# Performance work log

Measured on AMD Instinct MI355X. Metric: run time of the kernel, lower is better.

The kernel has to match this reference:

```python
import jax, jax.numpy as jnp
import numpy as np

N = 100000   # nodes
E = 3200000  # edges (avg degree 32)
F = 128      # feature dim
K = 10       # propagation order (hardcoded in module)


def setup_inputs() -> dict:
    key = jax.random.key(0)
    k1, k2 = jax.random.split(key, 2)
    x = jax.random.normal(k1, (N, F), dtype=jnp.float32)
    edge_index = jax.random.randint(k2, (2, E), 0, N, dtype=jnp.int32)
    mf_weights = jnp.ones((1, K + 1, 1), dtype=jnp.float32)
    # coef_upd='none' with alpha=0.5 -> lap_coefs init = min(1/0.5, 1.0) = 1.0, frozen
    lap_coefs = jnp.ones((K + 1,), dtype=jnp.float32)
    return {"x": x, "mf_weights": mf_weights, "lap_coefs": lap_coefs,
            "edge_index": edge_index}


def reference(x, mf_weights, lap_coefs, edge_index):
    n = x.shape[0]
    row, col = edge_index[0], edge_index[1]
    # gcn_norm without self loops: deg over destination (col), symmetric norm
    deg = jax.ops.segment_sum(jnp.ones((edge_index.shape[1],), x.dtype), col,
                              num_segments=n)
    dinv = jnp.where(deg > 0, jax.lax.rsqrt(jnp.maximum(deg, 1.0)) * jnp.where(deg > 0, jnp.ones_like(deg), 0.0), 0.0)
    dinv = jnp.where(deg > 0, deg ** -0.5, 0.0)
    norm = dinv[row] * dinv[col]  # [E]

    def prop(h):  # out[col] += norm * h[row]  (scatter-add SpMM)
        return jax.ops.segment_sum(norm[:, None] * h[row], col, num_segments=n)

    # Chebyshev-like recurrence: An=2, Bn=0, Cn=-1 -> P_i = 2*prop(P_{i-1}) - P_{i-2}
    outs = [x, prop(x)]
    for i in range(2, K + 1):
        outs.append(2.0 * prop(outs[-1]) - outs[-2])

    # coef_outs[0] = P0/1 ; coef_outs[i] = lap_coefs[i-1]/1 * P_i (norm_weights all 1)
    coef = jnp.concatenate([jnp.ones((1,), x.dtype), lap_coefs[:K]])  # [K+1]
    stacked = jnp.stack(outs, axis=1)  # [N, K+1, F]
    ret = jnp.sum(stacked * coef[None, :, None] * mf_weights, axis=1)  # [N, F]
    return ret
```

## Files before the change

kernel.cpp:

```cpp
#include <hip/hip_runtime.h>
#include <hip/hip_bf16.h>
#include <hip/hip_fp16.h>

#define FDIM 128


__global__ void degree_kernel(const int* __restrict__ col, int* __restrict__ deg, int E) {
    int e = blockIdx.x * blockDim.x + threadIdx.x;
    if (e < E) atomicAdd(&deg[col[e]], 1);
}

__global__ void dinv_kernel(const int* __restrict__ deg, float* __restrict__ dinv, int N) {
    int i = blockIdx.x * blockDim.x + threadIdx.x;
    if (i < N) {
        int d = deg[i];
        dinv[i] = (d > 0) ? rsqrtf((float)d) : 0.0f;
    }
}


__global__ void scan_blocks_kernel(const int* __restrict__ deg, int* __restrict__ rowptr,
                                   int* __restrict__ bsum, int N) {
    __shared__ int s[256];
    int t = threadIdx.x;
    int i = blockIdx.x * 256 + t;
    int v = (i < N) ? deg[i] : 0;
    s[t] = v;
    __syncthreads();
    for (int off = 1; off < 256; off <<= 1) {
        int add = (t >= off) ? s[t - off] : 0;
        __syncthreads();
        s[t] += add;
        __syncthreads();
    }
    if (i < N) rowptr[i] = s[t] - v;
    if (t == 255) bsum[blockIdx.x] = s[255];
}

__global__ void scan_bsums_kernel(int* __restrict__ bsum, int* __restrict__ boff, int nb) {
    __shared__ int s[512];
    int t = threadIdx.x;
    int v = (t < nb) ? bsum[t] : 0;
    s[t] = v;
    __syncthreads();
    for (int off = 1; off < 512; off <<= 1) {
        int add = (t >= off) ? s[t - off] : 0;
        __syncthreads();
        s[t] += add;
        __syncthreads();
    }
    if (t < nb) boff[t] = s[t] - v;
}

__global__ void add_offsets_kernel(int* __restrict__ rowptr, int* __restrict__ cursor,
                                   const int* __restrict__ boff, int N, int E) {
    int i = blockIdx.x * blockDim.x + threadIdx.x;
    if (i < N) {
        int v = rowptr[i] + boff[i >> 8];
        rowptr[i] = v;
        cursor[i] = v;
    }
    if (i == 0) rowptr[N] = E;
}


__global__ void place_kernel(const int* __restrict__ row, const int* __restrict__ col,
                             const float* __restrict__ dinv, int* __restrict__ cursor,
                             float2* __restrict__ edata, int E) {
    int e = blockIdx.x * blockDim.x + threadIdx.x;
    if (e < E) {
        int r = row[e], c = col[e];
        float w = dinv[r] * dinv[c];
        int pos = atomicAdd(&cursor[c], 1);
        edata[pos] = make_float2(__int_as_float(r), w);
    }
}


__global__ void init_out_kernel(const float4* __restrict__ x, const float* __restrict__ mf,
                                float4* __restrict__ out, long n4) {
    long i = (long)blockIdx.x * blockDim.x + threadIdx.x;
    if (i < n4) {
        float w = mf[0];
        float4 v = x[i];
        out[i] = make_float4(w * v.x, w * v.y, w * v.z, w * v.w);
    }
}


template <typename ST>
__global__ __launch_bounds__(256) void gather_prop_kernel(
        const float2* __restrict__ edata, const int* __restrict__ rowptr,
        const ST* __restrict__ src, const float* __restrict__ prev2,
        float* __restrict__ tgt, __half* __restrict__ tgth, float* __restrict__ out,
        const float* __restrict__ mf, const float* __restrict__ lap,
        int i_coef, float scale, float beta, int N) {
    int wid = blockIdx.x * 4 + (threadIdx.x >> 6);
    if (wid >= N) return;
    int lane = threadIdx.x & 63;
    int begin = rowptr[wid];
    int end = rowptr[wid + 1];
    float accx = 0.f, accy = 0.f;
    int laneoff = lane << 1;
    #pragma unroll 4
    for (int e = begin; e < end; ++e) {
        float2 ed = edata[e];
        int idx = __float_as_int(ed.x);
        float w = ed.y;
        float vx, vy;
        if constexpr (sizeof(ST) == 4) {
            const float2 v = *(const float2*)(src + ((long)idx << 7) + laneoff);
            vx = v.x; vy = v.y;
        } else {
            const __half2 v = *(const __half2*)(src + ((long)idx << 7) + laneoff);
            float2 vf = __half22float2(v);
            vx = vf.x; vy = vf.y;
        }
        accx += w * vx;
        accy += w * vy;
    }
    float coef = mf[i_coef] * lap[i_coef - 1];
    long o = ((long)wid << 7) + laneoff;
    float2 p = *(const float2*)(prev2 + o);
    float tx = scale * accx + beta * p.x;
    float ty = scale * accy + beta * p.y;
    *(float2*)(tgt + o) = make_float2(tx, ty);
    if (tgth) *(__half2*)(tgth + o) = __floats2half2_rn(tx, ty);
    float2 ov = *(const float2*)(out + o);
    ov.x += coef * tx;
    ov.y += coef * ty;
    *(float2*)(out + o) = ov;
}

extern "C" void kernel_launch(void* const* d_in, const int* in_sizes, int n_in,
                              void* d_out, int out_size, void* d_ws, size_t ws_size,
                              hipStream_t stream) {
    const float* x   = (const float*)d_in[0];
    const float* mf  = (const float*)d_in[1];
    const float* lap = (const float*)d_in[2];
    const int*   ei  = (const int*)d_in[3];
    float* out = (float*)d_out;

    const int  K  = in_sizes[1] - 1;
    const long NF = (long)in_sizes[0];
    const int  N  = (int)(NF / FDIM);
    const int  E  = in_sizes[3] / 2;
    const int* row = ei;
    const int* col = ei + E;

    char* wp = (char*)d_ws;
    float*  bufA   = (float*)wp;  wp += NF * sizeof(float);
    float*  bufB   = (float*)wp;  wp += NF * sizeof(float);
    __half* hbufA  = (__half*)wp; wp += NF * sizeof(__half);
    __half* hbufB  = (__half*)wp; wp += NF * sizeof(__half);
    float2* edata  = (float2*)wp; wp += (size_t)E * sizeof(float2);
    int*    rowptr = (int*)wp;    wp += (size_t)(N + 1) * sizeof(int);
    int*    cursor = (int*)wp;    wp += (size_t)N * sizeof(int);
    int*    deg    = (int*)wp;    wp += (size_t)N * sizeof(int);
    float*  dinv   = (float*)wp;  wp += (size_t)N * sizeof(float);
    int*    bsum   = (int*)wp;    wp += 512 * sizeof(int);
    int*    boff   = (int*)wp;    wp += 512 * sizeof(int);

    const int BT = 256;
    const long n4 = NF / 4;
    const int n4_blocks = (int)((n4 + BT - 1) / BT);
    const int e_blocks  = (E + BT - 1) / BT;
    const int n_blocks  = (N + BT - 1) / BT;

    hipMemsetAsync(deg, 0, (size_t)N * sizeof(int), stream);
    degree_kernel<<<e_blocks, BT, 0, stream>>>(col, deg, E);
    dinv_kernel<<<n_blocks, BT, 0, stream>>>(deg, dinv, N);
    scan_blocks_kernel<<<n_blocks, BT, 0, stream>>>(deg, rowptr, bsum, N);
    scan_bsums_kernel<<<1, 512, 0, stream>>>(bsum, boff, n_blocks);
    add_offsets_kernel<<<n_blocks, BT, 0, stream>>>(rowptr, cursor, boff, N, E);
    place_kernel<<<e_blocks, BT, 0, stream>>>(row, col, dinv, cursor, edata, E);

    init_out_kernel<<<n4_blocks, BT, 0, stream>>>((const float4*)x, mf, (float4*)out, n4);

    const int g_blocks = (N + 3) / 4;

    gather_prop_kernel<float><<<g_blocks, BT, 0, stream>>>(edata, rowptr, x, x,
                                                           bufA, hbufA, out, mf, lap,
                                                           1, 1.0f, 0.0f, N);
    for (int i = 2; i <= K; ++i) {
        const __half* srch  = (i % 2 == 0) ? hbufA : hbufB;
        float*        tgt   = (i % 2 == 0) ? bufB : bufA;
        __half*       tgth  = (i % 2 == 0) ? hbufB : hbufA;
        const float*  prev2 = (i == 2) ? x : (const float*)tgt;
        if (i == K) tgth = nullptr;
        gather_prop_kernel<__half><<<g_blocks, BT, 0, stream>>>(edata, rowptr, srch, prev2,
                                                                tgt, tgth, out, mf, lap,
                                                                i, 2.0f, -1.0f, N);
    }
}
```

Measured before the change: 1.937 ms.

## Split wavefront into four edge groups with 16-byte half loads per lane

The gather kernel now processes four edges at once per wavefront. Each 16-lane group loads a full 256-byte fp16 row using 16-byte vector loads, and the partial sums are combined with cross-lane shuffles. The first propagation also reads an fp16 copy of x, produced in the init kernel, instead of fp32 x. Epilogue loads and stores use nontemporal hints. This is meant to raise memory-level parallelism and cut per-edge instruction count, at the cost of shuffle reductions, idle lanes on ragged degree tails, and fp16 rounding of x in the first hop.

```diff
diff --git a/kernel.cpp b/kernel.cpp
--- a/kernel.cpp
+++ b/kernel.cpp
@@ -3,6 +3,8 @@
 #include <hip/hip_fp16.h>
 
 #define FDIM 128
+
+typedef float f4 __attribute__((ext_vector_type(4)));
 
 
 __global__ void degree_kernel(const int* __restrict__ col, int* __restrict__ deg, int E) {
@@ -78,58 +80,110 @@
 
 
 __global__ void init_out_kernel(const float4* __restrict__ x, const float* __restrict__ mf,
-                                float4* __restrict__ out, long n4) {
+                                float4* __restrict__ out, float4* __restrict__ hx, long n8) {
     long i = (long)blockIdx.x * blockDim.x + threadIdx.x;
-    if (i < n4) {
+    if (i < n8) {
         float w = mf[0];
-        float4 v = x[i];
-        out[i] = make_float4(w * v.x, w * v.y, w * v.z, w * v.w);
-    }
-}
-
-
-template <typename ST>
+        float4 a = x[2 * i];
+        float4 b = x[2 * i + 1];
+        out[2 * i]     = make_float4(w * a.x, w * a.y, w * a.z, w * a.w);
+        out[2 * i + 1] = make_float4(w * b.x, w * b.y, w * b.z, w * b.w);
+        __half2 h[4];
+        h[0] = __floats2half2_rn(a.x, a.y);
+        h[1] = __floats2half2_rn(a.z, a.w);
+        h[2] = __floats2half2_rn(b.x, b.y);
+        h[3] = __floats2half2_rn(b.z, b.w);
+        hx[i] = *(const float4*)h;
+    }
+}
+
+
 __global__ __launch_bounds__(256) void gather_prop_kernel(
         const float2* __restrict__ edata, const int* __restrict__ rowptr,
-        const ST* __restrict__ src, const float* __restrict__ prev2,
+        const __half* __restrict__ src, const float* __restrict__ prev2,
         float* __restrict__ tgt, __half* __restrict__ tgth, float* __restrict__ out,
         const float* __restrict__ mf, const float* __restrict__ lap,
         int i_coef, float scale, float beta, int N) {
     int wid = blockIdx.x * 4 + (threadIdx.x >> 6);
     if (wid >= N) return;
     int lane = threadIdx.x & 63;
+    int g  = lane >> 4;
+    int fl = lane & 15;
+    int feoff = fl << 3;
+
     int begin = rowptr[wid];
-    int end = rowptr[wid + 1];
-    float accx = 0.f, accy = 0.f;
-    int laneoff = lane << 1;
+    int end   = rowptr[wid + 1];
+
+    float acc[8];
+    #pragma unroll
+    for (int j = 0; j < 8; ++j) acc[j] = 0.f;
+
     #pragma unroll 4
-    for (int e = begin; e < end; ++e) {
-        float2 ed = edata[e];
-        int idx = __float_as_int(ed.x);
-        float w = ed.y;
-        float vx, vy;
-        if constexpr (sizeof(ST) == 4) {
-            const float2 v = *(const float2*)(src + ((long)idx << 7) + laneoff);
-            vx = v.x; vy = v.y;
+    for (int e0 = begin; e0 < end; e0 += 4) {
+        int e = e0 + g;
+        float w = 0.f;
+        int idx = 0;
+        if (e < end) {
+            float2 ed = edata[e];
+            idx = __float_as_int(ed.x);
+            w = ed.y;
+        }
+        f4 raw = *(const f4*)(src + ((long)idx << 7) + feoff);
+        const __half2* h = (const __half2*)&raw;
+        float2 f0 = __half22float2(h[0]);
+        float2 f1 = __half22float2(h[1]);
+        float2 f2 = __half22float2(h[2]);
+        float2 f3 = __half22float2(h[3]);
+        acc[0] += w * f0.x; acc[1] += w * f0.y;
+        acc[2] += w * f1.x; acc[3] += w * f1.y;
+        acc[4] += w * f2.x; acc[5] += w * f2.y;
+        acc[6] += w * f3.x; acc[7] += w * f3.y;
+    }
+
+    #pragma unroll
+    for (int j = 0; j < 8; ++j) {
+        acc[j] += __shfl_xor(acc[j], 16, 64);
+        acc[j] += __shfl_xor(acc[j], 32, 64);
+    }
+
+    if (g == 0) {
+        float coef = mf[i_coef] * lap[i_coef - 1];
+        long o = ((long)wid << 7) + feoff;
+        float r[8];
+        if (beta != 0.f) {
+            f4 p0 = __builtin_nontemporal_load((const f4*)(prev2 + o));
+            f4 p1 = __builtin_nontemporal_load((const f4*)(prev2 + o) + 1);
+            r[0] = scale * acc[0] + beta * p0.x;
+            r[1] = scale * acc[1] + beta * p0.y;
+            r[2] = scale * acc[2] + beta * p0.z;
+            r[3] = scale * acc[3] + beta * p0.w;
+            r[4] = scale * acc[4] + beta * p1.x;
+            r[5] = scale * acc[5] + beta * p1.y;
+            r[6] = scale * acc[6] + beta * p1.z;
+            r[7] = scale * acc[7] + beta * p1.w;
         } else {
-            const __half2 v = *(const __half2*)(src + ((long)idx << 7) + laneoff);
-            float2 vf = __half22float2(v);
-            vx = vf.x; vy = vf.y;
+            #pragma unroll
+            for (int j = 0; j < 8; ++j) r[j] = scale * acc[j];
         }
-        accx += w * vx;
-        accy += w * vy;
-    }
-    float coef = mf[i_coef] * lap[i_coef - 1];
-    long o = ((long)wid << 7) + laneoff;
-    float2 p = *(const float2*)(prev2 + o);
-    float tx = scale * accx + beta * p.x;
-    float ty = scale * accy + beta * p.y;
-    *(float2*)(tgt + o) = make_float2(tx, ty);
-    if (tgth) *(__half2*)(tgth + o) = __floats2half2_rn(tx, ty);
-    float2 ov = *(const float2*)(out + o);
-    ov.x += coef * tx;
-    ov.y += coef * ty;
-    *(float2*)(out + o) = ov;
+        f4 t0 = {r[0], r[1], r[2], r[3]};
+        f4 t1 = {r[4], r[5], r[6], r[7]};
+        __builtin_nontemporal_store(t0, (f4*)(tgt + o));
+        __builtin_nontemporal_store(t1, (f4*)(tgt + o) + 1);
+        if (tgth) {
+            __half2 hh[4];
+            hh[0] = __floats2half2_rn(r[0], r[1]);
+            hh[1] = __floats2half2_rn(r[2], r[3]);
+            hh[2] = __floats2half2_rn(r[4], r[5]);
+            hh[3] = __floats2half2_rn(r[6], r[7]);
+            __builtin_nontemporal_store(*(const f4*)hh, (f4*)(tgth + o));
+        }
+        f4 o0 = __builtin_nontemporal_load((const f4*)(out + o));
+        f4 o1 = __builtin_nontemporal_load((const f4*)(out + o) + 1);
+        o0.x += coef * r[0]; o0.y += coef * r[1]; o0.z += coef * r[2]; o0.w += coef * r[3];
+        o1.x += coef * r[4]; o1.y += coef * r[5]; o1.z += coef * r[6]; o1.w += coef * r[7];
+        __builtin_nontemporal_store(o0, (f4*)(out + o));
+        __builtin_nontemporal_store(o1, (f4*)(out + o) + 1);
+    }
 }
 
 extern "C" void kernel_launch(void* const* d_in, const int* in_sizes, int n_in,
@@ -162,8 +216,8 @@
     int*    boff   = (int*)wp;    wp += 512 * sizeof(int);
 
     const int BT = 256;
-    const long n4 = NF / 4;
-    const int n4_blocks = (int)((n4 + BT - 1) / BT);
+    const long n8 = NF / 8;
+    const int n8_blocks = (int)((n8 + BT - 1) / BT);
     const int e_blocks  = (E + BT - 1) / BT;
     const int n_blocks  = (N + BT - 1) / BT;
 
@@ -175,21 +229,22 @@
     add_offsets_kernel<<<n_blocks, BT, 0, stream>>>(rowptr, cursor, boff, N, E);
     place_kernel<<<e_blocks, BT, 0, stream>>>(row, col, dinv, cursor, edata, E);
 
-    init_out_kernel<<<n4_blocks, BT, 0, stream>>>((const float4*)x, mf, (float4*)out, n4);
+    init_out_kernel<<<n8_blocks, BT, 0, stream>>>((const float4*)x, mf, (float4*)out,
+                                                  (float4*)hbufB, n8);
 
     const int g_blocks = (N + 3) / 4;
 
-    gather_prop_kernel<float><<<g_blocks, BT, 0, stream>>>(edata, rowptr, x, x,
-                                                           bufA, hbufA, out, mf, lap,
-                                                           1, 1.0f, 0.0f, N);
+    gather_prop_kernel<<<g_blocks, BT, 0, stream>>>(edata, rowptr, hbufB, x,
+                                                    bufA, hbufA, out, mf, lap,
+                                                    1, 1.0f, 0.0f, N);
     for (int i = 2; i <= K; ++i) {
         const __half* srch  = (i % 2 == 0) ? hbufA : hbufB;
         float*        tgt   = (i % 2 == 0) ? bufB : bufA;
         __half*       tgth  = (i % 2 == 0) ? hbufB : hbufA;
         const float*  prev2 = (i == 2) ? x : (const float*)tgt;
         if (i == K) tgth = nullptr;
-        gather_prop_kernel<__half><<<g_blocks, BT, 0, stream>>>(edata, rowptr, srch, prev2,
-                                                                tgt, tgth, out, mf, lap,
-                                                                i, 2.0f, -1.0f, N);
-    }
-}
+        gather_prop_kernel<<<g_blocks, BT, 0, stream>>>(edata, rowptr, srch, prev2,
+                                                        tgt, tgth, out, mf, lap,
+                                                        i, 2.0f, -1.0f, N);
+    }
+}
```

Measured after the change: 1.783 ms. 7.9% less time.
